# Kernel tuning notes

Measured on AMD Instinct MI355X. Metric: run time of the kernel, lower is better.

Reference implementation:

```python
import jax, jax.numpy as jnp
import numpy as np

VOCAB, E, HID, HD, S, T = 50000, 1024, 1024, 512, 4096, 20
START, STOP, NEG = 18, 19, -10000.0


def setup_inputs() -> dict:
    key = jax.random.key(0)
    ks = jax.random.split(key, 16)
    scale = 0.05
    trans = jax.random.normal(ks[12], (T, T), jnp.float32)
    trans = trans.at[START, :].set(NEG).at[:, START].set(NEG)
    return {
        'sentence': jax.random.randint(ks[0], (S,), 0, VOCAB),
        'embed_table': jax.random.normal(ks[1], (VOCAB, E), jnp.float32) * scale,
        'w_ih_f': jax.random.normal(ks[2], (4 * HD, E), jnp.float32) * scale,
        'w_hh_f': jax.random.normal(ks[3], (4 * HD, HD), jnp.float32) * scale,
        'b_ih_f': jax.random.normal(ks[4], (4 * HD,), jnp.float32) * scale,
        'b_hh_f': jax.random.normal(ks[5], (4 * HD,), jnp.float32) * scale,
        'w_ih_b': jax.random.normal(ks[6], (4 * HD, E), jnp.float32) * scale,
        'w_hh_b': jax.random.normal(ks[7], (4 * HD, HD), jnp.float32) * scale,
        'b_ih_b': jax.random.normal(ks[8], (4 * HD,), jnp.float32) * scale,
        'b_hh_b': jax.random.normal(ks[9], (4 * HD,), jnp.float32) * scale,
        'w_out': jax.random.normal(ks[10], (T, HID), jnp.float32) * scale,
        'b_out': jax.random.normal(ks[11], (T,), jnp.float32) * scale,
        'transitions': trans,
        'h0': jax.random.normal(ks[13], (2, HD), jnp.float32),
        'c0': jax.random.normal(ks[14], (2, HD), jnp.float32),
    }


def _lstm_dir(pre, w_hh, b_hh, h0, c0, reverse):
    # pre: [S, 4HD] = x @ W_ih^T + b_ih (precomputed big GEMM)
    def step(carry, p):
        h, c = carry
        g = p + h @ w_hh.T + b_hh
        i, f, gg, o = jnp.split(g, 4, axis=-1)  # torch gate order i,f,g,o
        c = jax.nn.sigmoid(f) * c + jax.nn.sigmoid(i) * jnp.tanh(gg)
        h = jax.nn.sigmoid(o) * jnp.tanh(c)
        return (h, c), h
    _, hs = jax.lax.scan(step, (h0, c0), pre, reverse=reverse)
    return hs  # [S, HD], time-aligned in both directions


def _get_feats(sentence, embed_table, w_ih_f, w_hh_f, b_ih_f, b_hh_f,
               w_ih_b, w_hh_b, b_ih_b, b_hh_b, w_out, b_out, h0, c0):
    x = embed_table[sentence]                       # [S, E]
    hf = _lstm_dir(x @ w_ih_f.T + b_ih_f, w_hh_f, b_hh_f, h0[0], c0[0], False)
    hb = _lstm_dir(x @ w_ih_b.T + b_ih_b, w_hh_b, b_hh_b, h0[1], c0[1], True)
    lstm_out = jnp.concatenate([hf, hb], axis=-1)   # [S, HID]
    return lstm_out @ w_out.T + b_out               # [S, T]


def reference(sentence, embed_table, w_ih_f, w_hh_f, b_ih_f, b_hh_f,
              w_ih_b, w_hh_b, b_ih_b, b_hh_b, w_out, b_out,
              transitions, h0, c0):
    feats = _get_feats(sentence, embed_table, w_ih_f, w_hh_f, b_ih_f, b_hh_f,
                       w_ih_b, w_hh_b, b_ih_b, b_hh_b, w_out, b_out, h0, c0)
    # Viterbi decode
    init_v = jnp.full((T,), NEG, jnp.float32).at[START].set(0.0)

    def step(fv, feat):
        nt = fv[None, :] + transitions            # [T_cur, T_prev]
        best = jnp.argmax(nt, axis=1)             # backpointers [T]
        fv_new = jnp.max(nt, axis=1) + feat
        return fv_new, best

    fv_last, bptrs = jax.lax.scan(step, init_v, feats)
    terminal = fv_last + transitions[STOP]
    path_score = jnp.max(terminal)
    best_tag = jnp.argmax(terminal)

    def back(tag, bp):
        return bp[tag], tag
    _, path = jax.lax.scan(back, best_tag, bptrs, reverse=True)  # [S]
    return path_score, path
```

## Files before the change

### kernel.cpp

```cpp
#include <hip/hip_runtime.h>
#include <math.h>

#define S_LEN 4096
#define NTAG 20
#define TAG_STOP 19
#define NEGV -10000.0f


__global__ void init_ws(unsigned int* ready, unsigned long long* hpub) {
    int i = blockIdx.x * 256 + threadIdx.x;
    if (i < 64) ready[i] = 0u;
    if (i < 2048) hpub[i] = 0ull;
}

__device__ __forceinline__ float sigm(float x) { return 1.0f / (1.0f + expf(-x)); }

__device__ __forceinline__ unsigned long long agent_ld(const unsigned long long* p) {
    return __hip_atomic_load(p, __ATOMIC_RELAXED, __HIP_MEMORY_SCOPE_AGENT);
}

__device__ __forceinline__ void tile_wait(const unsigned int* ready, unsigned int& rdy_tile, int t) {
    if ((unsigned int)t != rdy_tile) {
        while (__hip_atomic_load(&ready[t], __ATOMIC_ACQUIRE, __HIP_MEMORY_SCOPE_AGENT) < 32u)
            __builtin_amdgcn_s_sleep(4);
        rdy_tile = (unsigned int)t;
    }
}

template<int P>
__device__ __forceinline__ void lstm_step(
    int s, int dir, int wg, int j, int ks, int su, bool own, int sidx, bool gate,
    const float* __restrict__ pre, const float* __restrict__ h0,
    float* __restrict__ hs, unsigned long long* pub,
    const unsigned int* __restrict__ ready, unsigned int& rdy_tile,
    float (&buf)[2][576],
    const float (&wr0)[32], const float (&wr1)[32],
    const float (&wr2)[32], const float (&wr3)[32],
    float (&pf)[4], float& c_reg)
{
    if (s == 0) {
        buf[0][sidx] = h0[dir * 512 + su];
    } else if (!own) {
        const unsigned int expect = (unsigned int)s;
        const unsigned long long* p = &pub[P * 512 + su];
        unsigned long long u = agent_ld(p);
        while ((unsigned int)(u >> 32) < expect) u = agent_ld(p);
        buf[P][sidx] = __uint_as_float((unsigned int)u);
    }
    __syncthreads();

    float a0 = 0.f, a1 = 0.f, a2 = 0.f, a3 = 0.f;
    const float* hp = &buf[P][ks * 36];
    #pragma unroll
    for (int q = 0; q < 8; ++q) {
        float4 h4 = ((const float4*)hp)[q];
        a0 += wr0[q*4+0]*h4.x + wr0[q*4+1]*h4.y + wr0[q*4+2]*h4.z + wr0[q*4+3]*h4.w;
        a1 += wr1[q*4+0]*h4.x + wr1[q*4+1]*h4.y + wr1[q*4+2]*h4.z + wr1[q*4+3]*h4.w;
        a2 += wr2[q*4+0]*h4.x + wr2[q*4+1]*h4.y + wr2[q*4+2]*h4.z + wr2[q*4+3]*h4.w;
        a3 += wr3[q*4+0]*h4.x + wr3[q*4+1]*h4.y + wr3[q*4+2]*h4.z + wr3[q*4+3]*h4.w;
    }
    a0 += __shfl_xor(a0, 1); a0 += __shfl_xor(a0, 2); a0 += __shfl_xor(a0, 4); a0 += __shfl_xor(a0, 8);
    a1 += __shfl_xor(a1, 1); a1 += __shfl_xor(a1, 2); a1 += __shfl_xor(a1, 4); a1 += __shfl_xor(a1, 8);
    a2 += __shfl_xor(a2, 1); a2 += __shfl_xor(a2, 2); a2 += __shfl_xor(a2, 4); a2 += __shfl_xor(a2, 8);
    a3 += __shfl_xor(a3, 1); a3 += __shfl_xor(a3, 2); a3 += __shfl_xor(a3, 4); a3 += __shfl_xor(a3, 8);

    if (gate) {
        float gi = a0 + pf[0], gf = a1 + pf[1], gg = a2 + pf[2], go = a3 + pf[3];
        float cn = sigm(gf) * c_reg + sigm(gi) * tanhf(gg);
        float hN = sigm(go) * tanhf(cn);
        c_reg = cn;
        const int pos = dir ? (S_LEN - 1 - s) : s;
        hs[((size_t)dir * S_LEN + pos) * 512 + j] = hN;
        buf[P ^ 1][j + 4 * wg] = hN;
        unsigned long long uv = ((unsigned long long)(unsigned int)(s + 1) << 32)
                              | (unsigned long long)__float_as_uint(hN);
        __hip_atomic_store(&pub[(P ^ 1) * 512 + j], uv,
                           __ATOMIC_RELAXED, __HIP_MEMORY_SCOPE_AGENT);
        if (s + 2 < S_LEN) {
            const int pp = dir ? (S_LEN - 3 - s) : (s + 2);
            tile_wait(ready, rdy_tile, pp >> 6);
            const float* pb = pre + (size_t)pp * 4096 + dir * 2048 + j;
            pf[0] = pb[0]; pf[1] = pb[512]; pf[2] = pb[1024]; pf[3] = pb[1536];
        }
    }
}

__launch_bounds__(512, 2)
__global__ void fused_kernel(const int* __restrict__ sent, const float* __restrict__ embed,
                             const float* __restrict__ wf, const float* __restrict__ wb,
                             const float* __restrict__ bihf, const float* __restrict__ bhhf,
                             const float* __restrict__ bihb, const float* __restrict__ bhhb,
                             float* __restrict__ pre,
                             const float* __restrict__ w_hh_f, const float* __restrict__ w_hh_b,
                             const float* __restrict__ h0, const float* __restrict__ c0,
                             float* __restrict__ hs, unsigned long long* __restrict__ h_pub,
                             unsigned int* __restrict__ ready)
{
    __shared__ float As[16][68];
    __shared__ float Bs[16][136];
    __shared__ int   srow[64];
    __shared__ float buf[2][576];
    const int tid = threadIdx.x;

    if (blockIdx.x >= 32) {
        const int gq = blockIdx.x - 32;
        const int q  = gq >> 5;
        const int bn = gq & 31;
        const int bm = (q & 1) ? (63 - (q >> 1)) : (q >> 1);
        const int pos0 = bm * 64, row0 = bn * 128;
        if (tid < 64) srow[tid] = sent[pos0 + tid];
        __syncthreads();

        const int ty = tid >> 5, tx = tid & 31;
        float acc[4][4];
        #pragma unroll
        for (int m = 0; m < 4; ++m)
            #pragma unroll
            for (int n = 0; n < 4; ++n) acc[m][n] = 0.f;

        for (int kt = 0; kt < 1024; kt += 16) {
            if (tid < 256) {
                int m = tid >> 2, kc = (tid & 3) * 4;
                float4 v = *(const float4*)(embed + (size_t)srow[m] * 1024 + kt + kc);
                As[kc+0][m] = v.x; As[kc+1][m] = v.y; As[kc+2][m] = v.z; As[kc+3][m] = v.w;
            }
            {
                int n = tid >> 2, kc = (tid & 3) * 4;
                int grow = row0 + n;
                const float* wsrc = (grow < 2048) ? (wf + (size_t)grow * 1024)
                                                  : (wb + (size_t)(grow - 2048) * 1024);
                float4 v = *(const float4*)(wsrc + kt + kc);
                Bs[kc+0][n] = v.x; Bs[kc+1][n] = v.y; Bs[kc+2][n] = v.z; Bs[kc+3][n] = v.w;
            }
            __syncthreads();
            #pragma unroll
            for (int kk = 0; kk < 16; ++kk) {
                float4 av = *(const float4*)&As[kk][ty * 4];
                float4 bv = *(const float4*)&Bs[kk][tx * 4];
                float a[4] = {av.x, av.y, av.z, av.w};
                float b[4] = {bv.x, bv.y, bv.z, bv.w};
                #pragma unroll
                for (int m = 0; m < 4; ++m)
                    #pragma unroll
                    for (int n = 0; n < 4; ++n) acc[m][n] += a[m] * b[n];
            }
            __syncthreads();
        }
        #pragma unroll
        for (int m = 0; m < 4; ++m) {
            int pos = pos0 + ty * 4 + m;
            #pragma unroll
            for (int n = 0; n < 4; ++n) {
                int grow = row0 + tx * 4 + n;
                float bias = (grow < 2048) ? (bihf[grow] + bhhf[grow])
                                           : (bihb[grow - 2048] + bhhb[grow - 2048]);
                __hip_atomic_store(&pre[(size_t)pos * 4096 + grow], acc[m][n] + bias,
                                   __ATOMIC_RELAXED, __HIP_MEMORY_SCOPE_AGENT);
            }
        }
        __syncthreads();
        if (tid == 0)
            __hip_atomic_fetch_add(&ready[bm], 1u, __ATOMIC_RELEASE, __HIP_MEMORY_SCOPE_AGENT);
        return;
    }

    const int dir  = blockIdx.x >> 4;
    const int wg   = blockIdx.x & 15;
    const int wv   = tid >> 6;
    const int lane = tid & 63;
    const int rg   = lane >> 4;
    const int ks   = lane & 15;
    const int j    = wg * 32 + wv * 4 + rg;
    const float* w_hh = dir ? w_hh_b : w_hh_f;

    float wr0[32], wr1[32], wr2[32], wr3[32];
    {
        const float* wbase = w_hh + (size_t)j * 512 + ks * 32;
        #pragma unroll
        for (int qq = 0; qq < 8; ++qq) {
            float4 v0 = *(const float4*)(wbase + 0 * 262144 + qq * 4);
            wr0[qq*4+0] = v0.x; wr0[qq*4+1] = v0.y; wr0[qq*4+2] = v0.z; wr0[qq*4+3] = v0.w;
            float4 v1 = *(const float4*)(wbase + 1 * 262144 + qq * 4);
            wr1[qq*4+0] = v1.x; wr1[qq*4+1] = v1.y; wr1[qq*4+2] = v1.z; wr1[qq*4+3] = v1.w;
            float4 v2 = *(const float4*)(wbase + 2 * 262144 + qq * 4);
            wr2[qq*4+0] = v2.x; wr2[qq*4+1] = v2.y; wr2[qq*4+2] = v2.z; wr2[qq*4+3] = v2.w;
            float4 v3 = *(const float4*)(wbase + 3 * 262144 + qq * 4);
            wr3[qq*4+0] = v3.x; wr3[qq*4+1] = v3.y; wr3[qq*4+2] = v3.z; wr3[qq*4+3] = v3.w;
        }
    }

    const bool gate = (ks == 0);
    unsigned int rdy_tile = 0xffffffffu;
    float c_reg = 0.f;
    float pfA[4] = {0,0,0,0}, pfB[4] = {0,0,0,0};
    if (gate) {
        c_reg = c0[dir * 512 + j];
        const int p0 = dir ? (S_LEN - 1) : 0;
        const int p1 = dir ? (S_LEN - 2) : 1;
        tile_wait(ready, rdy_tile, p0 >> 6);
        tile_wait(ready, rdy_tile, p1 >> 6);
        const float* b0 = pre + (size_t)p0 * 4096 + dir * 2048 + j;
        const float* b1 = pre + (size_t)p1 * 4096 + dir * 2048 + j;
        pfA[0] = b0[0]; pfA[1] = b0[512]; pfA[2] = b0[1024]; pfA[3] = b0[1536];
        pfB[0] = b1[0]; pfB[1] = b1[512]; pfB[2] = b1[1024]; pfB[3] = b1[1536];
    }

    const int  su   = tid;
    const bool own  = ((su >> 5) == wg);
    const int  sidx = su + ((su >> 5) << 2);
    unsigned long long* pub = h_pub + dir * 1024;

    for (int s = 0; s < S_LEN; s += 2) {
        lstm_step<0>(s,     dir, wg, j, ks, su, own, sidx, gate,
                     pre, h0, hs, pub, ready, rdy_tile, buf, wr0, wr1, wr2, wr3, pfA, c_reg);
        lstm_step<1>(s + 1, dir, wg, j, ks, su, own, sidx, gate,
                     pre, h0, hs, pub, ready, rdy_tile, buf, wr0, wr1, wr2, wr3, pfB, c_reg);
    }
}

__launch_bounds__(256)
__global__ void feats_kernel(const float* __restrict__ hs, const float* __restrict__ w_out,
                             const float* __restrict__ b_out, float* __restrict__ feats)
{
    const int pos = blockIdx.x;
    const int tid = threadIdx.x;
    __shared__ float hbuf[1024];
    __shared__ float red[160];
    {
        const float* hf = hs + (size_t)pos * 512;
        const float* hb = hs + ((size_t)S_LEN + pos) * 512;
        if (tid < 128) *(float4*)&hbuf[tid * 4]           = *(const float4*)&hf[tid * 4];
        else           *(float4*)&hbuf[512 + (tid-128)*4] = *(const float4*)&hb[(tid - 128) * 4];
    }
    __syncthreads();
    if (tid < 160) {
        int tag = tid >> 3, part = tid & 7;
        const float* wrow = w_out + (size_t)tag * 1024 + part * 128;
        const float* hrow = hbuf + part * 128;
        float sum = 0.f;
        #pragma unroll
        for (int q = 0; q < 32; ++q) {
            float4 a = ((const float4*)hrow)[q];
            float4 b = ((const float4*)wrow)[q];
            sum += a.x*b.x + a.y*b.y + a.z*b.z + a.w*b.w;
        }
        red[tid] = sum;
    }
    __syncthreads();
    if (tid < NTAG) {
        float sum = b_out[tid];
        #pragma unroll
        for (int pq = 0; pq < 8; ++pq) sum += red[tid * 8 + pq];
        feats[(size_t)pos * NTAG + tid] = sum;
    }
}

__launch_bounds__(256)
__global__ void viterbi_kernel(const float* __restrict__ feats, const float* __restrict__ trans,
                               unsigned char* __restrict__ bptr, float* __restrict__ out)
{
    __shared__ float feat_lds[64 * NTAG];
    __shared__ int sh_best;
    __shared__ unsigned char Mmap[8][NTAG];
    __shared__ unsigned char entry_s[8];
    const int tid = threadIdx.x;

    if (tid < 64) {
        const int lane = tid;
        const int i = (lane < NTAG) ? lane : (NTAG - 1);
        float trow[NTAG];
        #pragma unroll
        for (int jj = 0; jj < NTAG; ++jj) trow[jj] = trans[i * NTAG + jj];
        float fv[NTAG];
        #pragma unroll
        for (int jj = 0; jj < NTAG; ++jj) fv[jj] = (jj == 18) ? 0.f : NEGV;

        for (int blk = 0; blk < 64; ++blk) {
            #pragma unroll
            for (int q = 0; q < 20; ++q)
                feat_lds[q * 64 + lane] = feats[blk * 1280 + q * 64 + lane];
            for (int ss = 0; ss < 64; ++ss) {
                int s = blk * 64 + ss;
                float best = fv[0] + trow[0];
                int bj = 0;
                #pragma unroll
                for (int jj = 1; jj < NTAG; ++jj) {
                    float cand = fv[jj] + trow[jj];
                    if (cand > best) { best = cand; bj = jj; }
                }
                float fnew = best + feat_lds[ss * NTAG + i];
                if (lane < NTAG) bptr[s * NTAG + lane] = (unsigned char)bj;
                #pragma unroll
                for (int jj = 0; jj < NTAG; ++jj) fv[jj] = __shfl(fnew, jj);
            }
        }
        if (lane == 0) {
            float best = -1e30f; int bt = 0;
            for (int jj = 0; jj < NTAG; ++jj) {
                float t2 = fv[jj] + trans[TAG_STOP * NTAG + jj];
                if (t2 > best) { best = t2; bt = jj; }
            }
            out[0] = best;
            sh_best = bt;
        }
    }
    __syncthreads();
    if (tid < 160) {
        int c = tid / NTAG, e = tid % NTAG;
        int tag = e;
        for (int t = (c + 1) * 512 - 1; t >= c * 512; --t) tag = bptr[t * NTAG + tag];
        Mmap[c][e] = (unsigned char)tag;
    }
    __syncthreads();
    if (tid == 0) {
        int e = sh_best;
        entry_s[7] = (unsigned char)e;
        for (int c = 7; c >= 1; --c) { e = Mmap[c][e]; entry_s[c - 1] = (unsigned char)e; }
    }
    __syncthreads();
    if (tid < 8) {
        int c = tid;
        int tag = entry_s[c];
        out[1 + (c + 1) * 512 - 1] = (float)tag;
        for (int t = (c + 1) * 512 - 1; t > c * 512; --t) {
            tag = bptr[t * NTAG + tag];
            out[1 + t - 1] = (float)tag;
        }
    }
}

extern "C" void kernel_launch(void* const* d_in, const int* in_sizes, int n_in,
                              void* d_out, int out_size, void* d_ws, size_t ws_size,
                              hipStream_t stream) {
    (void)in_sizes; (void)n_in; (void)out_size; (void)ws_size;
    const int*   sent  = (const int*)d_in[0];
    const float* embed = (const float*)d_in[1];
    const float* wihf  = (const float*)d_in[2];
    const float* whhf  = (const float*)d_in[3];
    const float* bihf  = (const float*)d_in[4];
    const float* bhhf  = (const float*)d_in[5];
    const float* wihb  = (const float*)d_in[6];
    const float* whhb  = (const float*)d_in[7];
    const float* bihb  = (const float*)d_in[8];
    const float* bhhb  = (const float*)d_in[9];
    const float* wout  = (const float*)d_in[10];
    const float* bout  = (const float*)d_in[11];
    const float* trans = (const float*)d_in[12];
    const float* h0    = (const float*)d_in[13];
    const float* c0    = (const float*)d_in[14];

    char* ws = (char*)d_ws;
    unsigned int* ready       = (unsigned int*)ws;
    unsigned long long* h_pub = (unsigned long long*)(ws + 4096);
    float* pre   = (float*)(ws + 65536);
    float* hs    = (float*)(ws + 65536 + (size_t)4096 * 4096 * 4);
    float* feats = (float*)(ws + 65536 + (size_t)4096 * 4096 * 4 + (size_t)2 * 4096 * 512 * 4);
    unsigned char* bptr = (unsigned char*)(feats + (size_t)S_LEN * NTAG);
    float* out = (float*)d_out;

    hipLaunchKernelGGL(init_ws, dim3(8), dim3(256), 0, stream, ready, h_pub);
    hipLaunchKernelGGL(fused_kernel, dim3(32 + 2048), dim3(512), 0, stream,
                       sent, embed, wihf, wihb, bihf, bhhf, bihb, bhhb, pre,
                       whhf, whhb, h0, c0, hs, h_pub, ready);
    hipLaunchKernelGGL(feats_kernel, dim3(S_LEN), dim3(256), 0, stream,
                       hs, wout, bout, feats);
    hipLaunchKernelGGL(viterbi_kernel, dim3(1), dim3(256), 0, stream,
                       feats, trans, bptr, out);
}
```

Before: 10.35 ms.

## Move LSTM pre-activation prefetch and hs stores off the gate thread critical path

The recurrent LSTM loop now has the 32 owner threads of each workgroup prefetch the pre-activation gate inputs two steps ahead into a three-slot LDS ring. They also write the previous step's hidden state to global memory. This leaves the 16-lane gate thread doing only the nonlinearity and publish, which shortens the serial per-step latency. The Viterbi kernel also replaces its linear argmax with a tree reduction and splits the backtrace into 32 chunks over 1024 threads. The cost is extra LDS traffic and a dependence on correct slot indexing across the barrier.

```diff
diff --git a/kernel.cpp b/kernel.cpp
--- a/kernel.cpp
+++ b/kernel.cpp
@@ -24,64 +24,6 @@
         while (__hip_atomic_load(&ready[t], __ATOMIC_ACQUIRE, __HIP_MEMORY_SCOPE_AGENT) < 32u)
             __builtin_amdgcn_s_sleep(4);
         rdy_tile = (unsigned int)t;
-    }
-}
-
-template<int P>
-__device__ __forceinline__ void lstm_step(
-    int s, int dir, int wg, int j, int ks, int su, bool own, int sidx, bool gate,
-    const float* __restrict__ pre, const float* __restrict__ h0,
-    float* __restrict__ hs, unsigned long long* pub,
-    const unsigned int* __restrict__ ready, unsigned int& rdy_tile,
-    float (&buf)[2][576],
-    const float (&wr0)[32], const float (&wr1)[32],
-    const float (&wr2)[32], const float (&wr3)[32],
-    float (&pf)[4], float& c_reg)
-{
-    if (s == 0) {
-        buf[0][sidx] = h0[dir * 512 + su];
-    } else if (!own) {
-        const unsigned int expect = (unsigned int)s;
-        const unsigned long long* p = &pub[P * 512 + su];
-        unsigned long long u = agent_ld(p);
-        while ((unsigned int)(u >> 32) < expect) u = agent_ld(p);
-        buf[P][sidx] = __uint_as_float((unsigned int)u);
-    }
-    __syncthreads();
-
-    float a0 = 0.f, a1 = 0.f, a2 = 0.f, a3 = 0.f;
-    const float* hp = &buf[P][ks * 36];
-    #pragma unroll
-    for (int q = 0; q < 8; ++q) {
-        float4 h4 = ((const float4*)hp)[q];
-        a0 += wr0[q*4+0]*h4.x + wr0[q*4+1]*h4.y + wr0[q*4+2]*h4.z + wr0[q*4+3]*h4.w;
-        a1 += wr1[q*4+0]*h4.x + wr1[q*4+1]*h4.y + wr1[q*4+2]*h4.z + wr1[q*4+3]*h4.w;
-        a2 += wr2[q*4+0]*h4.x + wr2[q*4+1]*h4.y + wr2[q*4+2]*h4.z + wr2[q*4+3]*h4.w;
-        a3 += wr3[q*4+0]*h4.x + wr3[q*4+1]*h4.y + wr3[q*4+2]*h4.z + wr3[q*4+3]*h4.w;
-    }
-    a0 += __shfl_xor(a0, 1); a0 += __shfl_xor(a0, 2); a0 += __shfl_xor(a0, 4); a0 += __shfl_xor(a0, 8);
-    a1 += __shfl_xor(a1, 1); a1 += __shfl_xor(a1, 2); a1 += __shfl_xor(a1, 4); a1 += __shfl_xor(a1, 8);
-    a2 += __shfl_xor(a2, 1); a2 += __shfl_xor(a2, 2); a2 += __shfl_xor(a2, 4); a2 += __shfl_xor(a2, 8);
-    a3 += __shfl_xor(a3, 1); a3 += __shfl_xor(a3, 2); a3 += __shfl_xor(a3, 4); a3 += __shfl_xor(a3, 8);
-
-    if (gate) {
-        float gi = a0 + pf[0], gf = a1 + pf[1], gg = a2 + pf[2], go = a3 + pf[3];
-        float cn = sigm(gf) * c_reg + sigm(gi) * tanhf(gg);
-        float hN = sigm(go) * tanhf(cn);
-        c_reg = cn;
-        const int pos = dir ? (S_LEN - 1 - s) : s;
-        hs[((size_t)dir * S_LEN + pos) * 512 + j] = hN;
-        buf[P ^ 1][j + 4 * wg] = hN;
-        unsigned long long uv = ((unsigned long long)(unsigned int)(s + 1) << 32)
-                              | (unsigned long long)__float_as_uint(hN);
-        __hip_atomic_store(&pub[(P ^ 1) * 512 + j], uv,
-                           __ATOMIC_RELAXED, __HIP_MEMORY_SCOPE_AGENT);
-        if (s + 2 < S_LEN) {
-            const int pp = dir ? (S_LEN - 3 - s) : (s + 2);
-            tile_wait(ready, rdy_tile, pp >> 6);
-            const float* pb = pre + (size_t)pp * 4096 + dir * 2048 + j;
-            pf[0] = pb[0]; pf[1] = pb[512]; pf[2] = pb[1024]; pf[3] = pb[1536];
-        }
     }
 }
 
@@ -100,6 +42,7 @@
     __shared__ float Bs[16][136];
     __shared__ int   srow[64];
     __shared__ float buf[2][576];
+    __shared__ float pf_lds[3][32][4];
     const int tid = threadIdx.x;
 
     if (blockIdx.x >= 32) {
@@ -171,6 +114,7 @@
     const int rg   = lane >> 4;
     const int ks   = lane & 15;
     const int j    = wg * 32 + wv * 4 + rg;
+    const int lj   = wv * 4 + rg;
     const float* w_hh = dir ? w_hh_b : w_hh_f;
 
     float wr0[32], wr1[32], wr2[32], wr3[32];
@@ -190,31 +134,99 @@
     }
 
     const bool gate = (ks == 0);
+    const bool ownL = ((tid >> 5) == wg);
+    const int  lj2  = tid - wg * 32;
+    const int  su   = tid;
+    const bool own  = ownL;
+    const int  sidx = su + ((su >> 5) << 2);
+    unsigned long long* pub = h_pub + dir * 1024;
+
     unsigned int rdy_tile = 0xffffffffu;
     float c_reg = 0.f;
-    float pfA[4] = {0,0,0,0}, pfB[4] = {0,0,0,0};
-    if (gate) {
-        c_reg = c0[dir * 512 + j];
+    if (gate) c_reg = c0[dir * 512 + j];
+
+    if (ownL) {
         const int p0 = dir ? (S_LEN - 1) : 0;
         const int p1 = dir ? (S_LEN - 2) : 1;
         tile_wait(ready, rdy_tile, p0 >> 6);
+        const float* pb0 = pre + (size_t)p0 * 4096 + dir * 2048 + tid;
+        pf_lds[0][lj2][0] = pb0[0]; pf_lds[0][lj2][1] = pb0[512];
+        pf_lds[0][lj2][2] = pb0[1024]; pf_lds[0][lj2][3] = pb0[1536];
         tile_wait(ready, rdy_tile, p1 >> 6);
-        const float* b0 = pre + (size_t)p0 * 4096 + dir * 2048 + j;
-        const float* b1 = pre + (size_t)p1 * 4096 + dir * 2048 + j;
-        pfA[0] = b0[0]; pfA[1] = b0[512]; pfA[2] = b0[1024]; pfA[3] = b0[1536];
-        pfB[0] = b1[0]; pfB[1] = b1[512]; pfB[2] = b1[1024]; pfB[3] = b1[1536];
-    }
-
-    const int  su   = tid;
-    const bool own  = ((su >> 5) == wg);
-    const int  sidx = su + ((su >> 5) << 2);
-    unsigned long long* pub = h_pub + dir * 1024;
-
-    for (int s = 0; s < S_LEN; s += 2) {
-        lstm_step<0>(s,     dir, wg, j, ks, su, own, sidx, gate,
-                     pre, h0, hs, pub, ready, rdy_tile, buf, wr0, wr1, wr2, wr3, pfA, c_reg);
-        lstm_step<1>(s + 1, dir, wg, j, ks, su, own, sidx, gate,
-                     pre, h0, hs, pub, ready, rdy_tile, buf, wr0, wr1, wr2, wr3, pfB, c_reg);
+        const float* pb1 = pre + (size_t)p1 * 4096 + dir * 2048 + tid;
+        pf_lds[1][lj2][0] = pb1[0]; pf_lds[1][lj2][1] = pb1[512];
+        pf_lds[1][lj2][2] = pb1[1024]; pf_lds[1][lj2][3] = pb1[1536];
+    }
+
+    for (int s = 0; s < S_LEN; ++s) {
+        const int P = s & 1;
+        if (s == 0) {
+            buf[0][sidx] = h0[dir * 512 + su];
+        } else if (!own) {
+            const unsigned int expect = (unsigned int)s;
+            const unsigned long long* p = &pub[P * 512 + su];
+            unsigned long long u = agent_ld(p);
+            while ((unsigned int)(u >> 32) < expect) u = agent_ld(p);
+            buf[P][sidx] = __uint_as_float((unsigned int)u);
+        }
+        __syncthreads();
+
+        float4 pf4 = make_float4(0.f, 0.f, 0.f, 0.f);
+        if (gate) pf4 = *(const float4*)&pf_lds[s % 3][lj][0];
+
+        float pr0 = 0.f, pr1 = 0.f, pr2 = 0.f, pr3 = 0.f;
+        const bool doPre = ownL && (s + 2 < S_LEN);
+        if (doPre) {
+            const int pp = dir ? (S_LEN - 3 - s) : (s + 2);
+            tile_wait(ready, rdy_tile, pp >> 6);
+            const float* pb = pre + (size_t)pp * 4096 + dir * 2048 + tid;
+            pr0 = pb[0]; pr1 = pb[512]; pr2 = pb[1024]; pr3 = pb[1536];
+        }
+
+        float a0 = 0.f, a1 = 0.f, a2 = 0.f, a3 = 0.f;
+        const float* hp = &buf[P][ks * 36];
+        #pragma unroll
+        for (int q = 0; q < 8; ++q) {
+            float4 h4 = ((const float4*)hp)[q];
+            a0 += wr0[q*4+0]*h4.x + wr0[q*4+1]*h4.y + wr0[q*4+2]*h4.z + wr0[q*4+3]*h4.w;
+            a1 += wr1[q*4+0]*h4.x + wr1[q*4+1]*h4.y + wr1[q*4+2]*h4.z + wr1[q*4+3]*h4.w;
+            a2 += wr2[q*4+0]*h4.x + wr2[q*4+1]*h4.y + wr2[q*4+2]*h4.z + wr2[q*4+3]*h4.w;
+            a3 += wr3[q*4+0]*h4.x + wr3[q*4+1]*h4.y + wr3[q*4+2]*h4.z + wr3[q*4+3]*h4.w;
+        }
+        a0 += __shfl_xor(a0, 1); a0 += __shfl_xor(a0, 2); a0 += __shfl_xor(a0, 4); a0 += __shfl_xor(a0, 8);
+        a1 += __shfl_xor(a1, 1); a1 += __shfl_xor(a1, 2); a1 += __shfl_xor(a1, 4); a1 += __shfl_xor(a1, 8);
+        a2 += __shfl_xor(a2, 1); a2 += __shfl_xor(a2, 2); a2 += __shfl_xor(a2, 4); a2 += __shfl_xor(a2, 8);
+        a3 += __shfl_xor(a3, 1); a3 += __shfl_xor(a3, 2); a3 += __shfl_xor(a3, 4); a3 += __shfl_xor(a3, 8);
+
+        if (ownL) {
+            if (s > 0) {
+                float hv = buf[P][tid + 4 * wg];
+                const int posm = dir ? (S_LEN - s) : (s - 1);
+                hs[((size_t)dir * S_LEN + posm) * 512 + tid] = hv;
+            }
+            if (doPre) {
+                float* d = &pf_lds[(s + 2) % 3][lj2][0];
+                d[0] = pr0; d[1] = pr1; d[2] = pr2; d[3] = pr3;
+            }
+        }
+
+        if (gate) {
+            float gi = a0 + pf4.x, gf = a1 + pf4.y, gg = a2 + pf4.z, go = a3 + pf4.w;
+            float cn = sigm(gf) * c_reg + sigm(gi) * tanhf(gg);
+            float hN = sigm(go) * tanhf(cn);
+            c_reg = cn;
+            unsigned long long uv = ((unsigned long long)(unsigned int)(s + 1) << 32)
+                                  | (unsigned long long)__float_as_uint(hN);
+            __hip_atomic_store(&pub[(P ^ 1) * 512 + j], uv,
+                               __ATOMIC_RELAXED, __HIP_MEMORY_SCOPE_AGENT);
+            buf[P ^ 1][j + 4 * wg] = hN;
+        }
+    }
+    __syncthreads();
+    if (ownL) {
+        float hv = buf[0][tid + 4 * wg];
+        const int posm = dir ? 0 : (S_LEN - 1);
+        hs[((size_t)dir * S_LEN + posm) * 512 + tid] = hv;
     }
 }
 
@@ -255,14 +267,14 @@
     }
 }
 
-__launch_bounds__(256)
+__launch_bounds__(1024)
 __global__ void viterbi_kernel(const float* __restrict__ feats, const float* __restrict__ trans,
                                unsigned char* __restrict__ bptr, float* __restrict__ out)
 {
     __shared__ float feat_lds[64 * NTAG];
     __shared__ int sh_best;
-    __shared__ unsigned char Mmap[8][NTAG];
-    __shared__ unsigned char entry_s[8];
+    __shared__ unsigned char Mmap[32][NTAG];
+    __shared__ unsigned char entry_s[32];
     const int tid = threadIdx.x;
 
     if (tid < 64) {
@@ -281,15 +293,16 @@
                 feat_lds[q * 64 + lane] = feats[blk * 1280 + q * 64 + lane];
             for (int ss = 0; ss < 64; ++ss) {
                 int s = blk * 64 + ss;
-                float best = fv[0] + trow[0];
-                int bj = 0;
+                float cand[NTAG]; int idx[NTAG];
                 #pragma unroll
-                for (int jj = 1; jj < NTAG; ++jj) {
-                    float cand = fv[jj] + trow[jj];
-                    if (cand > best) { best = cand; bj = jj; }
-                }
-                float fnew = best + feat_lds[ss * NTAG + i];
-                if (lane < NTAG) bptr[s * NTAG + lane] = (unsigned char)bj;
+                for (int jj = 0; jj < NTAG; ++jj) { cand[jj] = fv[jj] + trow[jj]; idx[jj] = jj; }
+                #pragma unroll
+                for (int st = 1; st < NTAG; st <<= 1)
+                    #pragma unroll
+                    for (int j0 = 0; j0 + st < NTAG; j0 += 2 * st)
+                        if (cand[j0] < cand[j0 + st]) { cand[j0] = cand[j0 + st]; idx[j0] = idx[j0 + st]; }
+                float fnew = cand[0] + feat_lds[ss * NTAG + i];
+                if (lane < NTAG) bptr[s * NTAG + lane] = (unsigned char)idx[0];
                 #pragma unroll
                 for (int jj = 0; jj < NTAG; ++jj) fv[jj] = __shfl(fnew, jj);
             }
@@ -305,24 +318,24 @@
         }
     }
     __syncthreads();
-    if (tid < 160) {
+    if (tid < 32 * NTAG) {
         int c = tid / NTAG, e = tid % NTAG;
         int tag = e;
-        for (int t = (c + 1) * 512 - 1; t >= c * 512; --t) tag = bptr[t * NTAG + tag];
+        for (int t = (c + 1) * 128 - 1; t >= c * 128; --t) tag = bptr[t * NTAG + tag];
         Mmap[c][e] = (unsigned char)tag;
     }
     __syncthreads();
     if (tid == 0) {
         int e = sh_best;
-        entry_s[7] = (unsigned char)e;
-        for (int c = 7; c >= 1; --c) { e = Mmap[c][e]; entry_s[c - 1] = (unsigned char)e; }
-    }
-    __syncthreads();
-    if (tid < 8) {
+        entry_s[31] = (unsigned char)e;
+        for (int c = 31; c >= 1; --c) { e = Mmap[c][e]; entry_s[c - 1] = (unsigned char)e; }
+    }
+    __syncthreads();
+    if (tid < 32) {
         int c = tid;
         int tag = entry_s[c];
-        out[1 + (c + 1) * 512 - 1] = (float)tag;
-        for (int t = (c + 1) * 512 - 1; t > c * 512; --t) {
+        out[1 + (c + 1) * 128 - 1] = (float)tag;
+        for (int t = (c + 1) * 128 - 1; t > c * 128; --t) {
             tag = bptr[t * NTAG + tag];
             out[1 + t - 1] = (float)tag;
         }
@@ -364,6 +377,6 @@
                        whhf, whhb, h0, c0, hs, h_pub, ready);
     hipLaunchKernelGGL(feats_kernel, dim3(S_LEN), dim3(256), 0, stream,
                        hs, wout, bout, feats);
-    hipLaunchKernelGGL(viterbi_kernel, dim3(1), dim3(256), 0, stream,
+    hipLaunchKernelGGL(viterbi_kernel, dim3(1), dim3(1024), 0, stream,
                        feats, trans, bptr, out);
 }
```

Result: slower. 10.65 ms (+2.8%).
